# Optimization experiments

Hardware: AMD Instinct MI355X
Metric: run time of the kernel (lower is better)

The kernel has to match this reference:

```python
import jax, jax.numpy as jnp
import numpy as np
import math

B, S, D, H, L, V = 2, 2048, 1024, 16, 2, 32000
HD = D // H          # head_dim = 64
FF = 4 * D           # ffn hidden = 4096
NEG_INF = -1e9


def setup_inputs() -> dict:
    key = jax.random.key(0)
    ks = jax.random.split(key, 12)
    w = lambda k, shape: jax.random.normal(k, shape, dtype=jnp.float32) * 0.02
    return {
        "tokens": jax.random.randint(ks[0], (B, S), 0, V),
        "tok_emb": w(ks[1], (V, D)),
        "pos_emb": w(ks[2], (S, D)),
        # torch nn.Linear weights are [out, in]; stacked over layers
        "wq": w(ks[3], (L, D, D)),
        "wk": w(ks[4], (L, D, D)),
        "wv": w(ks[5], (L, D, D)),
        "wo": w(ks[6], (L, D, D)),
        "w1": w(ks[7], (L, FF, D)),
        "w2": w(ks[8], (L, D, FF)),
        "ln1_g": jnp.ones((L, D)), "ln1_b": jnp.zeros((L, D)),
        "ln2_g": jnp.ones((L, D)), "ln2_b": jnp.zeros((L, D)),
        "lnf_g": jnp.ones((D,)), "lnf_b": jnp.zeros((D,)),
        "w_out": w(ks[9], (V, D)),
    }


def _layernorm(x, g, b):
    m = jnp.mean(x, axis=-1, keepdims=True)
    v = jnp.mean(jnp.square(x - m), axis=-1, keepdims=True)
    return (x - m) * jax.lax.rsqrt(v + 1e-5) * g + b


def _transformer(tokens, tok_emb, pos_emb, wq, wk, wv, wo, w1, w2,
                 ln1_g, ln1_b, ln2_g, ln2_b, lnf_g, lnf_b, w_out):
    s = tokens.shape[1]
    # causal additive mask [1,1,S,S]
    mask = jnp.where(jnp.tril(jnp.ones((s, s), dtype=bool)), 0.0, NEG_INF)[None, None]
    h = tok_emb[tokens] + pos_emb[None, :s]
    scale = 1.0 / math.sqrt(HD)
    for l in range(L):
        # pre-norm attention
        a_in = _layernorm(h, ln1_g[l], ln1_b[l])
        q = (a_in @ wq[l].T).reshape(B, s, H, HD)
        k = (a_in @ wk[l].T).reshape(B, s, H, HD)
        v = (a_in @ wv[l].T).reshape(B, s, H, HD)
        scores = jnp.einsum('bqhd,bkhd->bhqk', q, k) * scale + mask
        attn = jax.nn.softmax(scores.astype(jnp.float32), axis=-1).astype(h.dtype)
        o = jnp.einsum('bhqk,bkhd->bqhd', attn, v).reshape(B, s, D)
        h = h + o @ wo[l].T
        # pre-norm ReLU FFN
        f_in = _layernorm(h, ln2_g[l], ln2_b[l])
        h = h + jax.nn.relu(f_in @ w1[l].T) @ w2[l].T
    h = _layernorm(h, lnf_g, lnf_b)
    return h @ w_out.T  # [B,S,V]


def reference(tokens, tok_emb, pos_emb, wq, wk, wv, wo, w1, w2,
              ln1_g, ln1_b, ln2_g, ln2_b, lnf_g, lnf_b, w_out):
    return _transformer(tokens, tok_emb, pos_emb, wq, wk, wv, wo, w1, w2,
                        ln1_g, ln1_b, ln2_g, ln2_b, lnf_g, lnf_b, w_out)
```

## Files before the change

### kernel.cpp

```cpp
#include <hip/hip_runtime.h>

#define Bv 2
#define Sv 2048
#define Dv 1024
#define Hv 16
#define HDv 64
#define FFv 4096
#define Vv 32000

typedef short bf16x8 __attribute__((ext_vector_type(8)));
typedef float f32x4 __attribute__((ext_vector_type(4)));
typedef unsigned short us8 __attribute__((ext_vector_type(8)));
typedef unsigned short us4 __attribute__((ext_vector_type(4)));
typedef unsigned short u16;

__device__ __forceinline__ u16 f2bf(float f) {
  union { float f; unsigned u; } x; x.f = f;
  x.u += 0x7fffu + ((x.u >> 16) & 1u);
  return (u16)(x.u >> 16);
}
__device__ __forceinline__ u16 f2bf_rtz(float f) {
  union { float f; unsigned u; } x; x.f = f;
  return (u16)(x.u >> 16);
}

__device__ __forceinline__ void gld16(const void* g, void* l) {
  __builtin_amdgcn_global_load_lds(
      (const __attribute__((address_space(1))) unsigned*)g,
      (__attribute__((address_space(3))) unsigned*)l, 16, 0, 0);
}

__global__ __launch_bounds__(256) void k_embed(const int* __restrict__ tok,
    const float* __restrict__ te, const float* __restrict__ pe,
    float* __restrict__ h) {
  int row = blockIdx.x;
  int s = row & (Sv - 1);
  int t = tok[row];
  float4 va = ((const float4*)(te + (size_t)t * Dv))[threadIdx.x];
  float4 vb = ((const float4*)(pe + (size_t)s * Dv))[threadIdx.x];
  float4 o;
  o.x = va.x + vb.x; o.y = va.y + vb.y; o.z = va.z + vb.z; o.w = va.w + vb.w;
  ((float4*)(h + (size_t)row * Dv))[threadIdx.x] = o;
}

__global__ __launch_bounds__(256) void k_cvt(const float* __restrict__ x,
    u16* __restrict__ y, int n4) {
  int i = blockIdx.x * 256 + threadIdx.x;
  if (i >= n4) return;
  float4 v = ((const float4*)x)[i];
  us4 o = { f2bf(v.x), f2bf(v.y), f2bf(v.z), f2bf(v.w) };
  ((us4*)y)[i] = o;
}

__global__ __launch_bounds__(256) void k_ln(const float* __restrict__ x,
    const float* __restrict__ g, const float* __restrict__ bb,
    u16* __restrict__ y) {
  int row = blockIdx.x, t = threadIdx.x;
  float4 v = ((const float4*)(x + (size_t)row * Dv))[t];
  float s = v.x + v.y + v.z + v.w;
#pragma unroll
  for (int m = 32; m; m >>= 1) s += __shfl_xor(s, m, 64);
  __shared__ float red[4];
  if ((t & 63) == 0) red[t >> 6] = s;
  __syncthreads();
  float mean = (red[0] + red[1] + red[2] + red[3]) * (1.0f / Dv);
  __syncthreads();
  float dx = v.x - mean, dy = v.y - mean, dz = v.z - mean, dw = v.w - mean;
  float s2 = dx * dx + dy * dy + dz * dz + dw * dw;
#pragma unroll
  for (int m = 32; m; m >>= 1) s2 += __shfl_xor(s2, m, 64);
  if ((t & 63) == 0) red[t >> 6] = s2;
  __syncthreads();
  float var = (red[0] + red[1] + red[2] + red[3]) * (1.0f / Dv);
  float rstd = rsqrtf(var + 1e-5f);
  float4 gg = ((const float4*)g)[t];
  float4 be = ((const float4*)bb)[t];
  us4 o = { f2bf(dx * rstd * gg.x + be.x), f2bf(dy * rstd * gg.y + be.y),
            f2bf(dz * rstd * gg.z + be.z), f2bf(dw * rstd * gg.w + be.w) };
  ((us4*)(y + (size_t)row * Dv))[t] = o;
}

__device__ __forceinline__ void stage32(const u16* __restrict__ g, int ldK,
    u16* lds, int row_base, int kt, int lane) {
  int row = row_base + (lane >> 2);
  int slot = (lane & 3) ^ ((row >> 1) & 3);
  const u16* src = g + (size_t)row * ldK + (kt << 5) + (slot << 3);
  gld16(src, lds + (row_base << 5));
}
__device__ __forceinline__ bf16x8 ldfragA(const u16* lds, int row, int ks) {
  return *(const bf16x8*)((const char*)lds + row * 64 + ((ks ^ ((row >> 1) & 3)) << 4));
}

__device__ __forceinline__ void stage64(const u16* __restrict__ g, int ldK,
    u16* lds, int row_base, int kt, int lane) {
  int row = row_base + (lane >> 3);
  int slot = (lane & 7) ^ (row & 7);
  const u16* src = g + (size_t)row * ldK + (kt << 6) + (slot << 3);
  gld16(src, lds + (row_base << 6));
}
__device__ __forceinline__ bf16x8 ldf64(const u16* lds, int row, int slot) {
  return *(const bf16x8*)((const char*)lds + row * 128 + ((slot ^ (row & 7)) << 4));
}

template <int EPI>
__global__ __launch_bounds__(512, 2) void k_256(const u16* __restrict__ A,
    const u16* __restrict__ Bm, const float* __restrict__ res,
    float* __restrict__ Cf, u16* __restrict__ Cb, int M, int N, int K) {
  __shared__ u16 As[2][256 * 64];
  __shared__ u16 Bs[2][256 * 64];
  int TM = M >> 8, TN = N >> 8, nwg = TM * TN;
  int orig = blockIdx.x;
  int qd = nwg >> 3, rm = nwg & 7, xcd = orig & 7;
  int wg = (xcd < rm ? xcd * (qd + 1) : rm * (qd + 1) + (xcd - rm) * qd) + (orig >> 3);
  int bm = wg % TM, bn = wg / TM;
  int m0 = bm << 8, n0 = bn << 8;
  int lane = threadIdx.x & 63, wid = threadIdx.x >> 6;
  int wr = wid >> 2, wc = wid & 3;
  int NT = K >> 6;
  const u16* Ag = A + (size_t)m0 * K;
  const u16* Bg = Bm + (size_t)n0 * K;
  int frow = lane & 15, ks = lane >> 4;

  f32x4 acc[8][4] = {};
  bf16x8 af[4], bk0[4], bk1[4];

#pragma unroll
  for (int tt = 0; tt < 2; tt++) {
#pragma unroll
    for (int j = 0; j < 4; j++) stage64(Ag, K, As[tt], wid * 32 + j * 8, tt, lane);
#pragma unroll
    for (int j = 0; j < 4; j++) stage64(Bg, K, Bs[tt], wid * 32 + j * 8, tt, lane);
  }
  asm volatile("s_waitcnt vmcnt(8)" ::: "memory");
  __builtin_amdgcn_s_barrier();

  for (int t = 0; t < NT; t++) {
    int p = t & 1;
    const u16* Ab = As[p];
    const u16* Bb = Bs[p];
#pragma unroll
    for (int f = 0; f < 4; f++) af[f] = ldf64(Ab, wr * 128 + f * 16 + frow, ks);
#pragma unroll
    for (int n = 0; n < 4; n++) bk0[n] = ldf64(Bb, wc * 64 + n * 16 + frow, ks);
    __builtin_amdgcn_s_barrier();
    asm volatile("s_waitcnt lgkmcnt(0)" ::: "memory");
    __builtin_amdgcn_sched_barrier(0);
    __builtin_amdgcn_s_setprio(1);
#pragma unroll
    for (int f = 0; f < 4; f++)
#pragma unroll
      for (int n = 0; n < 4; n++)
        acc[f][n] = __builtin_amdgcn_mfma_f32_16x16x32_bf16(af[f], bk0[n], acc[f][n], 0, 0, 0);
    __builtin_amdgcn_s_setprio(0);
    __builtin_amdgcn_sched_barrier(0);
    __builtin_amdgcn_s_barrier();
#pragma unroll
    for (int f = 0; f < 4; f++) af[f] = ldf64(Ab, wr * 128 + 64 + f * 16 + frow, ks);
#pragma unroll
    for (int n = 0; n < 4; n++) bk1[n] = ldf64(Bb, wc * 64 + n * 16 + frow, 4 + ks);
    __builtin_amdgcn_s_barrier();
    asm volatile("s_waitcnt lgkmcnt(0)" ::: "memory");
    __builtin_amdgcn_sched_barrier(0);
    __builtin_amdgcn_s_setprio(1);
#pragma unroll
    for (int f = 0; f < 4; f++)
#pragma unroll
      for (int n = 0; n < 4; n++)
        acc[4 + f][n] = __builtin_amdgcn_mfma_f32_16x16x32_bf16(af[f], bk0[n], acc[4 + f][n], 0, 0, 0);
    __builtin_amdgcn_s_setprio(0);
    __builtin_amdgcn_sched_barrier(0);
    __builtin_amdgcn_s_barrier();
#pragma unroll
    for (int f = 0; f < 4; f++) af[f] = ldf64(Ab, wr * 128 + f * 16 + frow, 4 + ks);
    __builtin_amdgcn_s_barrier();
    asm volatile("s_waitcnt lgkmcnt(0)" ::: "memory");
    __builtin_amdgcn_sched_barrier(0);
    __builtin_amdgcn_s_setprio(1);
#pragma unroll
    for (int f = 0; f < 4; f++)
#pragma unroll
      for (int n = 0; n < 4; n++)
        acc[f][n] = __builtin_amdgcn_mfma_f32_16x16x32_bf16(af[f], bk1[n], acc[f][n], 0, 0, 0);
    __builtin_amdgcn_s_setprio(0);
    __builtin_amdgcn_sched_barrier(0);
    __builtin_amdgcn_s_barrier();
#pragma unroll
    for (int f = 0; f < 4; f++) af[f] = ldf64(Ab, wr * 128 + 64 + f * 16 + frow, 4 + ks);
    __builtin_amdgcn_s_barrier();
    asm volatile("s_waitcnt lgkmcnt(0)" ::: "memory");
    __builtin_amdgcn_sched_barrier(0);
    __builtin_amdgcn_s_setprio(1);
#pragma unroll
    for (int f = 0; f < 4; f++)
#pragma unroll
      for (int n = 0; n < 4; n++)
        acc[4 + f][n] = __builtin_amdgcn_mfma_f32_16x16x32_bf16(af[f], bk1[n], acc[4 + f][n], 0, 0, 0);
    __builtin_amdgcn_s_setprio(0);
    __builtin_amdgcn_sched_barrier(0);
    __builtin_amdgcn_s_barrier();
    if (t + 2 < NT) {
#pragma unroll
      for (int j = 0; j < 4; j++) stage64(Ag, K, As[p], wid * 32 + j * 8, t + 2, lane);
#pragma unroll
      for (int j = 0; j < 4; j++) stage64(Bg, K, Bs[p], wid * 32 + j * 8, t + 2, lane);
      asm volatile("s_waitcnt vmcnt(8)" ::: "memory");
    } else {
      asm volatile("s_waitcnt vmcnt(0)" ::: "memory");
    }
    __builtin_amdgcn_s_barrier();
  }

#pragma unroll
  for (int f = 0; f < 8; f++) {
#pragma unroll
    for (int r = 0; r < 4; r++) {
      int row = m0 + wr * 128 + f * 16 + (lane >> 4) * 4 + r;
#pragma unroll
      for (int n = 0; n < 4; n++) {
        int col = n0 + wc * 64 + n * 16 + frow;
        float val = acc[f][n][r];
        size_t idx = (size_t)row * N + col;
        if constexpr (EPI == 1) { Cf[idx] = val + res[idx]; }
        else if constexpr (EPI == 0) { __builtin_nontemporal_store(val, &Cf[idx]); }
        else if constexpr (EPI == 2) { Cb[idx] = f2bf(val); }
        else { Cb[idx] = f2bf(fmaxf(val, 0.0f)); }
      }
    }
  }
}

template <int EPI>
__global__ __launch_bounds__(512, 4) void k_gemm8(const u16* __restrict__ A,
    const u16* __restrict__ Bm, const float* __restrict__ res,
    float* __restrict__ Cf, u16* __restrict__ Cb, int M, int N, int K) {
  __shared__ u16 As[2][128 * 32];
  __shared__ u16 Bs[2][256 * 32];
  int TM = M >> 7, TN = N >> 8, nwg = TM * TN;
  int orig = blockIdx.x;
  int qd = nwg >> 3, rm = nwg & 7, xcd = orig & 7;
  int wg = (xcd < rm ? xcd * (qd + 1) : rm * (qd + 1) + (xcd - rm) * qd) + (orig >> 3);
  int bm = wg % TM, bn = wg / TM;
  int m0 = bm << 7, n0 = bn << 8;
  int lane = threadIdx.x & 63, wid = threadIdx.x >> 6;
  int wr = wid >> 2, wc = wid & 3;
  int NT = K >> 5;
  const u16* Ag = A + (size_t)m0 * K;
  const u16* Bg = Bm + (size_t)n0 * K;
  int frow = lane & 15, ks = lane >> 4;

  f32x4 acc[4][4] = {};
  bf16x8 af[4], bf[4];

#pragma unroll
  for (int tt = 0; tt < 2; tt++) {
    stage32(Ag, K, As[tt], wid * 16, tt, lane);
    stage32(Bg, K, Bs[tt], wid * 32, tt, lane);
    stage32(Bg, K, Bs[tt], wid * 32 + 16, tt, lane);
  }
  asm volatile("s_waitcnt vmcnt(3)" ::: "memory");
  __builtin_amdgcn_s_barrier();

  for (int t = 0; t < NT; t++) {
    int p = t & 1;
    const u16* Ab = As[p];
    const u16* Bb = Bs[p];
#pragma unroll
    for (int f = 0; f < 4; f++) af[f] = ldfragA(Ab, wr * 64 + f * 16 + frow, ks);
#pragma unroll
    for (int n = 0; n < 4; n++) bf[n] = ldfragA(Bb, wc * 64 + n * 16 + frow, ks);
    __builtin_amdgcn_s_barrier();
    asm volatile("s_waitcnt lgkmcnt(0)" ::: "memory");
    __builtin_amdgcn_sched_barrier(0);
    __builtin_amdgcn_s_setprio(1);
#pragma unroll
    for (int f = 0; f < 2; f++)
#pragma unroll
      for (int n = 0; n < 4; n++)
        acc[f][n] = __builtin_amdgcn_mfma_f32_16x16x32_bf16(af[f], bf[n], acc[f][n], 0, 0, 0);
    __builtin_amdgcn_s_setprio(0);
    __builtin_amdgcn_sched_barrier(0);
    __builtin_amdgcn_s_barrier();
    if (t < NT - 2) {
      stage32(Ag, K, As[p], wid * 16, t + 2, lane);
      stage32(Bg, K, Bs[p], wid * 32, t + 2, lane);
      stage32(Bg, K, Bs[p], wid * 32 + 16, t + 2, lane);
    }
    __builtin_amdgcn_s_setprio(1);
#pragma unroll
    for (int f = 0; f < 2; f++)
#pragma unroll
      for (int n = 0; n < 4; n++)
        acc[2 + f][n] = __builtin_amdgcn_mfma_f32_16x16x32_bf16(af[2 + f], bf[n], acc[2 + f][n], 0, 0, 0);
    __builtin_amdgcn_s_setprio(0);
    __builtin_amdgcn_sched_barrier(0);
    if (t < NT - 2) { asm volatile("s_waitcnt vmcnt(3)" ::: "memory"); }
    else            { asm volatile("s_waitcnt vmcnt(0)" ::: "memory"); }
    __builtin_amdgcn_s_barrier();
  }

#pragma unroll
  for (int f = 0; f < 4; f++) {
#pragma unroll
    for (int r = 0; r < 4; r++) {
      int row = m0 + wr * 64 + f * 16 + (lane >> 4) * 4 + r;
#pragma unroll
      for (int n = 0; n < 4; n++) {
        int col = n0 + wc * 64 + n * 16 + frow;
        float val = acc[f][n][r];
        size_t idx = (size_t)row * N + col;
        if constexpr (EPI == 1) { Cf[idx] = val + res[idx]; }
        else if constexpr (EPI == 0) { __builtin_nontemporal_store(val, &Cf[idx]); }
        else if constexpr (EPI == 2) { Cb[idx] = f2bf(val); }
        else { Cb[idx] = f2bf(fmaxf(val, 0.0f)); }
      }
    }
  }
}

template <int EPI>
__global__ __launch_bounds__(256, 4) void k_gemmv(const u16* __restrict__ A,
    const u16* __restrict__ Bm, const float* __restrict__ res,
    float* __restrict__ Cf, u16* __restrict__ Cb, int M, int N, int K) {
  __shared__ u16 As[2][128 * 32];
  __shared__ u16 Bs[2][128 * 32];
  int TM = M >> 7, TN = N >> 7, nwg = TM * TN;
  int orig = blockIdx.x;
  int qd = nwg >> 3, rm = nwg & 7, xcd = orig & 7;
  int wg = (xcd < rm ? xcd * (qd + 1) : rm * (qd + 1) + (xcd - rm) * qd) + (orig >> 3);
  int bm = wg % TM, bn = wg / TM;
  int m0 = bm << 7, n0 = bn << 7;
  int lane = threadIdx.x & 63, wid = threadIdx.x >> 6;
  int wr = wid >> 1, wc = wid & 1;
  int NT = K >> 5;
  const u16* Ag = A + (size_t)m0 * K;
  const u16* Bg = Bm + (size_t)n0 * K;
  int frow = lane & 15, ks = lane >> 4;

  f32x4 acc[4][4] = {};
  bf16x8 af[4], bf[4];

#pragma unroll
  for (int tt = 0; tt < 2; tt++) {
    stage32(Ag, K, As[tt], wid * 32, tt, lane);
    stage32(Ag, K, As[tt], wid * 32 + 16, tt, lane);
    stage32(Bg, K, Bs[tt], wid * 32, tt, lane);
    stage32(Bg, K, Bs[tt], wid * 32 + 16, tt, lane);
  }
  asm volatile("s_waitcnt vmcnt(4)" ::: "memory");
  __builtin_amdgcn_s_barrier();

  for (int t = 0; t < NT; t++) {
    int p = t & 1;
    const u16* Ab = As[p];
    const u16* Bb = Bs[p];
#pragma unroll
    for (int f = 0; f < 4; f++) af[f] = ldfragA(Ab, wr * 64 + f * 16 + frow, ks);
#pragma unroll
    for (int n = 0; n < 4; n++) bf[n] = ldfragA(Bb, wc * 64 + n * 16 + frow, ks);
    __builtin_amdgcn_s_barrier();
    asm volatile("s_waitcnt lgkmcnt(0)" ::: "memory");
    __builtin_amdgcn_sched_barrier(0);
    __builtin_amdgcn_s_setprio(1);
#pragma unroll
    for (int f = 0; f < 2; f++)
#pragma unroll
      for (int n = 0; n < 4; n++)
        acc[f][n] = __builtin_amdgcn_mfma_f32_16x16x32_bf16(af[f], bf[n], acc[f][n], 0, 0, 0);
    __builtin_amdgcn_s_setprio(0);
    __builtin_amdgcn_sched_barrier(0);
    __builtin_amdgcn_s_barrier();
    if (t < NT - 2) {
      stage32(Ag, K, As[p], wid * 32, t + 2, lane);
      stage32(Ag, K, As[p], wid * 32 + 16, t + 2, lane);
      stage32(Bg, K, Bs[p], wid * 32, t + 2, lane);
      stage32(Bg, K, Bs[p], wid * 32 + 16, t + 2, lane);
    }
    __builtin_amdgcn_s_setprio(1);
#pragma unroll
    for (int f = 0; f < 2; f++)
#pragma unroll
      for (int n = 0; n < 4; n++)
        acc[2 + f][n] = __builtin_amdgcn_mfma_f32_16x16x32_bf16(af[2 + f], bf[n], acc[2 + f][n], 0, 0, 0);
    __builtin_amdgcn_s_setprio(0);
    __builtin_amdgcn_sched_barrier(0);
    if (t < NT - 2) { asm volatile("s_waitcnt vmcnt(4)" ::: "memory"); }
    else            { asm volatile("s_waitcnt vmcnt(0)" ::: "memory"); }
    __builtin_amdgcn_s_barrier();
  }

#pragma unroll
  for (int f = 0; f < 4; f++) {
#pragma unroll
    for (int r = 0; r < 4; r++) {
      int row = m0 + wr * 64 + f * 16 + (lane >> 4) * 4 + r;
#pragma unroll
      for (int n = 0; n < 4; n++) {
        int col = n0 + wc * 64 + n * 16 + frow;
        float val = acc[f][n][r];
        size_t idx = (size_t)row * N + col;
        if constexpr (EPI == 1) { Cf[idx] = val + res[idx]; }
        else if constexpr (EPI == 0) { __builtin_nontemporal_store(val, &Cf[idx]); }
        else if constexpr (EPI == 2) { Cb[idx] = f2bf(val); }
        else { Cb[idx] = f2bf(fmaxf(val, 0.0f)); }
      }
    }
  }
}

__global__ __launch_bounds__(256) void k_transpose(const u16* __restrict__ v,
    u16* __restrict__ vt, int stride) {
  int st = blockIdx.x & 31;
  int bh = blockIdx.x >> 5;
  int b = bh >> 4, hh = bh & 15;
  __shared__ u16 tile[64][72];
  int t = threadIdx.x;
  int rr = t >> 3, cc = (t & 7) << 3;
#pragma unroll
  for (int it = 0; it < 2; it++) {
    int r = rr + it * 32;
    us8 val = *(const us8*)(v + (size_t)(b * Sv + st * 64 + r) * stride + hh * HDv + cc);
    *(us8*)&tile[r][cc] = val;
  }
  __syncthreads();
#pragma unroll
  for (int it = 0; it < 2; it++) {
    int d = rr + it * 32;
    us8 val;
#pragma unroll
    for (int j = 0; j < 8; j++) val[j] = tile[cc + j][d];
    *(us8*)(vt + ((size_t)bh * HDv + d) * Sv + st * 64 + cc) = val;
  }
}

__global__ __launch_bounds__(256) void k_attn(const u16* __restrict__ qg,
    const u16* __restrict__ kg, const u16* __restrict__ vt,
    u16* __restrict__ og) {
  int qt = blockIdx.x & 15;
  int bh = blockIdx.x >> 4;
  int b = bh >> 4, hh = bh & 15;
  int wv = threadIdx.x >> 6, lane = threadIdx.x & 63;
  int q0 = qt * 128 + wv * 32;
  __shared__ u16 plds_s[4][32 * 40];
  __shared__ float alds_s[4][2][16];
  u16* plds = plds_s[wv];
  float (*alds)[16] = alds_s[wv];
  const int QS = 3 * Dv;
  const float scale = 0.125f;
  int qcol = lane & 15, g = lane >> 4;

  bf16x8 qf[2][2];
#pragma unroll
  for (int fm = 0; fm < 2; fm++)
#pragma unroll
    for (int dh = 0; dh < 2; dh++)
      qf[fm][dh] = *(const bf16x8*)(qg + (size_t)(b * Sv + q0 + fm * 16 + qcol) * QS
                                    + hh * HDv + dh * 32 + g * 8);

  f32x4 oacc[2][4] = {};
  float mrun[2] = { -1e30f, -1e30f };
  float lrun[2] = { 0.0f, 0.0f };

  int ktmax = (q0 + 31) >> 5;
  for (int kt = 0; kt <= ktmax; kt++) {
    int k0 = kt * 32;
    bf16x8 kf[2][2];
#pragma unroll
    for (int kn = 0; kn < 2; kn++)
#pragma unroll
      for (int dh = 0; dh < 2; dh++)
        kf[kn][dh] = *(const bf16x8*)(kg + (size_t)(b * Sv + k0 + kn * 16 + qcol) * QS
                                      + hh * HDv + dh * 32 + g * 8);
    f32x4 sa[2][2] = {};
#pragma unroll
    for (int dh = 0; dh < 2; dh++)
#pragma unroll
      for (int fm = 0; fm < 2; fm++)
#pragma unroll
        for (int kn = 0; kn < 2; kn++)
          sa[fm][kn] = __builtin_amdgcn_mfma_f32_16x16x32_bf16(kf[kn][dh], qf[fm][dh], sa[fm][kn], 0, 0, 0);

    bool full = (k0 + 31 <= q0);
#pragma unroll
    for (int fm = 0; fm < 2; fm++) {
      int qrow = q0 + fm * 16 + qcol;
      float s[2][4];
#pragma unroll
      for (int kn = 0; kn < 2; kn++)
#pragma unroll
        for (int r = 0; r < 4; r++) {
          float v = sa[fm][kn][r] * scale;
          if (!full && (k0 + kn * 16 + g * 4 + r) > qrow) v = -1e30f;
          s[kn][r] = v;
        }
      float rmx = s[0][0];
#pragma unroll
      for (int kn = 0; kn < 2; kn++)
#pragma unroll
        for (int r = 0; r < 4; r++) rmx = fmaxf(rmx, s[kn][r]);
      rmx = fmaxf(rmx, __shfl_xor(rmx, 16, 64));
      rmx = fmaxf(rmx, __shfl_xor(rmx, 32, 64));
      float nm;
      if (__all(rmx - mrun[fm] <= 8.0f)) {
        nm = mrun[fm];
      } else {
        nm = fmaxf(mrun[fm], rmx);
        float alpha = __expf(mrun[fm] - nm);
        mrun[fm] = nm;
        lrun[fm] *= alpha;
        if (g == 0) alds[fm][qcol] = alpha;
#pragma unroll
        for (int r = 0; r < 4; r++) {
          float al = alds[fm][g * 4 + r];
#pragma unroll
          for (int dn = 0; dn < 4; dn++) oacc[fm][dn][r] *= al;
        }
      }
      float rs = 0.0f;
      float pv[2][4];
#pragma unroll
      for (int kn = 0; kn < 2; kn++)
#pragma unroll
        for (int r = 0; r < 4; r++) { pv[kn][r] = __expf(s[kn][r] - nm); rs += pv[kn][r]; }
      rs += __shfl_xor(rs, 16, 64);
      rs += __shfl_xor(rs, 32, 64);
      lrun[fm] += rs;
#pragma unroll
      for (int kn = 0; kn < 2; kn++) {
        us4 pk = { f2bf_rtz(pv[kn][0]), f2bf_rtz(pv[kn][1]),
                   f2bf_rtz(pv[kn][2]), f2bf_rtz(pv[kn][3]) };
        *(us4*)(plds + (fm * 16 + qcol) * 40 + kn * 16 + g * 4) = pk;
      }
    }
    bf16x8 pf[2];
#pragma unroll
    for (int fm = 0; fm < 2; fm++)
      pf[fm] = *(const bf16x8*)(plds + (fm * 16 + qcol) * 40 + g * 8);
    bf16x8 vf[4];
#pragma unroll
    for (int dn = 0; dn < 4; dn++)
      vf[dn] = *(const bf16x8*)(vt + ((size_t)bh * HDv + dn * 16 + qcol) * Sv
                                + k0 + g * 8);
#pragma unroll
    for (int fm = 0; fm < 2; fm++)
#pragma unroll
      for (int dn = 0; dn < 4; dn++)
        oacc[fm][dn] = __builtin_amdgcn_mfma_f32_16x16x32_bf16(pf[fm], vf[dn], oacc[fm][dn], 0, 0, 0);
  }

#pragma unroll
  for (int fm = 0; fm < 2; fm++)
    if (g == 0) alds[fm][qcol] = 1.0f / lrun[fm];
#pragma unroll
  for (int fm = 0; fm < 2; fm++)
#pragma unroll
    for (int r = 0; r < 4; r++) {
      float li = alds[fm][g * 4 + r];
      int row = q0 + fm * 16 + g * 4 + r;
#pragma unroll
      for (int dn = 0; dn < 4; dn++)
        og[(size_t)(b * Sv + row) * Dv + hh * HDv + dn * 16 + qcol] =
            f2bf(oacc[fm][dn][r] * li);
    }
}

extern "C" void kernel_launch(void* const* d_in, const int* in_sizes, int n_in,
                              void* d_out, int out_size, void* d_ws, size_t ws_size,
                              hipStream_t stream) {
  const int*   tok  = (const int*)d_in[0];
  const float* te   = (const float*)d_in[1];
  const float* pe   = (const float*)d_in[2];
  const float* wq   = (const float*)d_in[3];
  const float* wk   = (const float*)d_in[4];
  const float* wvv  = (const float*)d_in[5];
  const float* wo   = (const float*)d_in[6];
  const float* w1   = (const float*)d_in[7];
  const float* w2   = (const float*)d_in[8];
  const float* ln1g = (const float*)d_in[9];
  const float* ln1b = (const float*)d_in[10];
  const float* ln2g = (const float*)d_in[11];
  const float* ln2b = (const float*)d_in[12];
  const float* lnfg = (const float*)d_in[13];
  const float* lnfb = (const float*)d_in[14];
  const float* wout = (const float*)d_in[15];
  float* out = (float*)d_out;

  char* p = (char*)d_ws;
  float* h  = (float*)p; p += (size_t)4096 * 1024 * 4;
  u16* a    = (u16*)p;   p += (size_t)4096 * 1024 * 2;
  u16* qkv  = (u16*)p;   p += (size_t)4096 * 3072 * 2;
  u16* vt   = (u16*)p;   p += (size_t)32 * 64 * 2048 * 2;
  u16* o    = (u16*)p;   p += (size_t)4096 * 1024 * 2;
  u16* f1   = (u16*)p;   p += (size_t)4096 * 4096 * 2;
  u16* wb   = (u16*)p;   p += (size_t)32000 * 1024 * 2;

  const int M = Bv * Sv;

  k_embed<<<M, 256, 0, stream>>>(tok, te, pe, h);
  for (int l = 0; l < 2; l++) {
    k_ln<<<M, 256, 0, stream>>>(h, ln1g + l * Dv, ln1b + l * Dv, a);
    k_cvt<<<1024, 256, 0, stream>>>(wq  + (size_t)l * Dv * Dv, wb,              (Dv * Dv) / 4);
    k_cvt<<<1024, 256, 0, stream>>>(wk  + (size_t)l * Dv * Dv, wb + Dv * Dv,    (Dv * Dv) / 4);
    k_cvt<<<1024, 256, 0, stream>>>(wvv + (size_t)l * Dv * Dv, wb + 2 * Dv * Dv,(Dv * Dv) / 4);
    k_gemm8<2><<<32 * 12, 512, 0, stream>>>(a, wb, nullptr, nullptr, qkv, M, 3 * Dv, Dv);
    k_transpose<<<1024, 256, 0, stream>>>(qkv + 2 * Dv, vt, 3 * Dv);
    k_attn<<<512, 256, 0, stream>>>(qkv, qkv + Dv, vt, o);
    k_cvt<<<1024, 256, 0, stream>>>(wo + (size_t)l * Dv * Dv, wb, (Dv * Dv) / 4);
    k_gemmv<1><<<32 * 8, 256, 0, stream>>>(o, wb, h, h, nullptr, M, Dv, Dv);
    k_ln<<<M, 256, 0, stream>>>(h, ln2g + l * Dv, ln2b + l * Dv, a);
    k_cvt<<<4096, 256, 0, stream>>>(w1 + (size_t)l * FFv * Dv, wb, (FFv * Dv) / 4);
    k_256<3><<<16 * 16, 512, 0, stream>>>(a, wb, nullptr, nullptr, f1, M, FFv, Dv);
    k_cvt<<<4096, 256, 0, stream>>>(w2 + (size_t)l * Dv * FFv, wb, (Dv * FFv) / 4);
    k_gemmv<1><<<32 * 8, 256, 0, stream>>>(f1, wb, h, h, nullptr, M, Dv, FFv);
  }
  k_ln<<<M, 256, 0, stream>>>(h, lnfg, lnfb, a);
  k_cvt<<<32000, 256, 0, stream>>>(wout, wb, (Vv * Dv) / 4);
  k_256<0><<<16 * 125, 512, 0, stream>>>(a, wb, nullptr, out, nullptr, M, Vv, Dv);
}
```

Before: 1.075 ms.

## Restructure 256x256 GEMM main loop to batch LDS reads and prefetch earlier

The per-tile loop of the large bf16 GEMM (used for the FFN up-projection and the vocabulary projection) is rewritten. Most LDS fragment loads for all four MFMA sub-blocks are now issued up front into separate registers, and most intermediate workgroup barriers are removed. The global prefetch of tile t+2 is moved before the last MFMA block so that it overlaps with compute. The aim is to cut barrier and LDS-latency stalls, at the cost of many more live fragment registers, which may add register pressure or spills under launch_bounds(512,2).

```diff
diff --git a/kernel.cpp b/kernel.cpp
--- a/kernel.cpp
+++ b/kernel.cpp
@@ -103,7 +103,7 @@
 }
 
 template <int EPI>
-__global__ __launch_bounds__(512, 2) void k_256(const u16* __restrict__ A,
+__global__ __launch_bounds__(512, 2) void k_pipe(const u16* __restrict__ A,
     const u16* __restrict__ Bm, const float* __restrict__ res,
     float* __restrict__ Cf, u16* __restrict__ Cb, int M, int N, int K) {
   __shared__ u16 As[2][256 * 64];
@@ -122,7 +122,7 @@
   int frow = lane & 15, ks = lane >> 4;
 
   f32x4 acc[8][4] = {};
-  bf16x8 af[4], bk0[4], bk1[4];
+  bf16x8 af0[4], af1[4], af2[4], af3[4], bf0[4], bf1[4];
 
 #pragma unroll
   for (int tt = 0; tt < 2; tt++) {
@@ -139,74 +139,57 @@
     const u16* Ab = As[p];
     const u16* Bb = Bs[p];
 #pragma unroll
-    for (int f = 0; f < 4; f++) af[f] = ldf64(Ab, wr * 128 + f * 16 + frow, ks);
-#pragma unroll
-    for (int n = 0; n < 4; n++) bk0[n] = ldf64(Bb, wc * 64 + n * 16 + frow, ks);
-    __builtin_amdgcn_s_barrier();
+    for (int f = 0; f < 4; f++) af0[f] = ldf64(Ab, wr * 128 + f * 16 + frow, ks);
+#pragma unroll
+    for (int n = 0; n < 4; n++) bf0[n] = ldf64(Bb, wc * 64 + n * 16 + frow, ks);
+#pragma unroll
+    for (int f = 0; f < 4; f++) af1[f] = ldf64(Ab, wr * 128 + 64 + f * 16 + frow, ks);
+#pragma unroll
+    for (int n = 0; n < 4; n++) bf1[n] = ldf64(Bb, wc * 64 + n * 16 + frow, 4 + ks);
+#pragma unroll
+    for (int f = 0; f < 4; f++) af2[f] = ldf64(Ab, wr * 128 + f * 16 + frow, 4 + ks);
+    __builtin_amdgcn_s_setprio(1);
+#pragma unroll
+    for (int f = 0; f < 4; f++)
+#pragma unroll
+      for (int n = 0; n < 4; n++)
+        acc[f][n] = __builtin_amdgcn_mfma_f32_16x16x32_bf16(af0[f], bf0[n], acc[f][n], 0, 0, 0);
+    __builtin_amdgcn_s_setprio(0);
+    __builtin_amdgcn_s_setprio(1);
+#pragma unroll
+    for (int f = 0; f < 4; f++)
+#pragma unroll
+      for (int n = 0; n < 4; n++)
+        acc[4 + f][n] = __builtin_amdgcn_mfma_f32_16x16x32_bf16(af1[f], bf0[n], acc[4 + f][n], 0, 0, 0);
+    __builtin_amdgcn_s_setprio(0);
+#pragma unroll
+    for (int f = 0; f < 4; f++) af3[f] = ldf64(Ab, wr * 128 + 64 + f * 16 + frow, 4 + ks);
+    __builtin_amdgcn_s_setprio(1);
+#pragma unroll
+    for (int f = 0; f < 4; f++)
+#pragma unroll
+      for (int n = 0; n < 4; n++)
+        acc[f][n] = __builtin_amdgcn_mfma_f32_16x16x32_bf16(af2[f], bf1[n], acc[f][n], 0, 0, 0);
+    __builtin_amdgcn_s_setprio(0);
     asm volatile("s_waitcnt lgkmcnt(0)" ::: "memory");
     __builtin_amdgcn_sched_barrier(0);
+    __builtin_amdgcn_s_barrier();
+    if (t + 2 < NT) {
+#pragma unroll
+      for (int j = 0; j < 4; j++) stage64(Ag, K, As[p], wid * 32 + j * 8, t + 2, lane);
+#pragma unroll
+      for (int j = 0; j < 4; j++) stage64(Bg, K, Bs[p], wid * 32 + j * 8, t + 2, lane);
+    }
     __builtin_amdgcn_s_setprio(1);
 #pragma unroll
     for (int f = 0; f < 4; f++)
 #pragma unroll
       for (int n = 0; n < 4; n++)
-        acc[f][n] = __builtin_amdgcn_mfma_f32_16x16x32_bf16(af[f], bk0[n], acc[f][n], 0, 0, 0);
-    __builtin_amdgcn_s_setprio(0);
-    __builtin_amdgcn_sched_barrier(0);
-    __builtin_amdgcn_s_barrier();
-#pragma unroll
-    for (int f = 0; f < 4; f++) af[f] = ldf64(Ab, wr * 128 + 64 + f * 16 + frow, ks);
-#pragma unroll
-    for (int n = 0; n < 4; n++) bk1[n] = ldf64(Bb, wc * 64 + n * 16 + frow, 4 + ks);
-    __builtin_amdgcn_s_barrier();
-    asm volatile("s_waitcnt lgkmcnt(0)" ::: "memory");
-    __builtin_amdgcn_sched_barrier(0);
-    __builtin_amdgcn_s_setprio(1);
-#pragma unroll
-    for (int f = 0; f < 4; f++)
-#pragma unroll
-      for (int n = 0; n < 4; n++)
-        acc[4 + f][n] = __builtin_amdgcn_mfma_f32_16x16x32_bf16(af[f], bk0[n], acc[4 + f][n], 0, 0, 0);
-    __builtin_amdgcn_s_setprio(0);
-    __builtin_amdgcn_sched_barrier(0);
-    __builtin_amdgcn_s_barrier();
-#pragma unroll
-    for (int f = 0; f < 4; f++) af[f] = ldf64(Ab, wr * 128 + f * 16 + frow, 4 + ks);
-    __builtin_amdgcn_s_barrier();
-    asm volatile("s_waitcnt lgkmcnt(0)" ::: "memory");
-    __builtin_amdgcn_sched_barrier(0);
-    __builtin_amdgcn_s_setprio(1);
-#pragma unroll
-    for (int f = 0; f < 4; f++)
-#pragma unroll
-      for (int n = 0; n < 4; n++)
-        acc[f][n] = __builtin_amdgcn_mfma_f32_16x16x32_bf16(af[f], bk1[n], acc[f][n], 0, 0, 0);
-    __builtin_amdgcn_s_setprio(0);
-    __builtin_amdgcn_sched_barrier(0);
-    __builtin_amdgcn_s_barrier();
-#pragma unroll
-    for (int f = 0; f < 4; f++) af[f] = ldf64(Ab, wr * 128 + 64 + f * 16 + frow, 4 + ks);
-    __builtin_amdgcn_s_barrier();
-    asm volatile("s_waitcnt lgkmcnt(0)" ::: "memory");
-    __builtin_amdgcn_sched_barrier(0);
-    __builtin_amdgcn_s_setprio(1);
-#pragma unroll
-    for (int f = 0; f < 4; f++)
-#pragma unroll
-      for (int n = 0; n < 4; n++)
-        acc[4 + f][n] = __builtin_amdgcn_mfma_f32_16x16x32_bf16(af[f], bk1[n], acc[4 + f][n], 0, 0, 0);
-    __builtin_amdgcn_s_setprio(0);
-    __builtin_amdgcn_sched_barrier(0);
-    __builtin_amdgcn_s_barrier();
-    if (t + 2 < NT) {
-#pragma unroll
-      for (int j = 0; j < 4; j++) stage64(Ag, K, As[p], wid * 32 + j * 8, t + 2, lane);
-#pragma unroll
-      for (int j = 0; j < 4; j++) stage64(Bg, K, Bs[p], wid * 32 + j * 8, t + 2, lane);
-      asm volatile("s_waitcnt vmcnt(8)" ::: "memory");
-    } else {
-      asm volatile("s_waitcnt vmcnt(0)" ::: "memory");
-    }
+        acc[4 + f][n] = __builtin_amdgcn_mfma_f32_16x16x32_bf16(af3[f], bf1[n], acc[4 + f][n], 0, 0, 0);
+    __builtin_amdgcn_s_setprio(0);
+    __builtin_amdgcn_sched_barrier(0);
+    if (t + 2 < NT) { asm volatile("s_waitcnt vmcnt(8)" ::: "memory"); }
+    else            { asm volatile("s_waitcnt vmcnt(0)" ::: "memory"); }
     __builtin_amdgcn_s_barrier();
   }
 
@@ -608,11 +591,11 @@
     k_gemmv<1><<<32 * 8, 256, 0, stream>>>(o, wb, h, h, nullptr, M, Dv, Dv);
     k_ln<<<M, 256, 0, stream>>>(h, ln2g + l * Dv, ln2b + l * Dv, a);
     k_cvt<<<4096, 256, 0, stream>>>(w1 + (size_t)l * FFv * Dv, wb, (FFv * Dv) / 4);
-    k_256<3><<<16 * 16, 512, 0, stream>>>(a, wb, nullptr, nullptr, f1, M, FFv, Dv);
+    k_pipe<3><<<16 * 16, 512, 0, stream>>>(a, wb, nullptr, nullptr, f1, M, FFv, Dv);
     k_cvt<<<4096, 256, 0, stream>>>(w2 + (size_t)l * Dv * FFv, wb, (Dv * FFv) / 4);
     k_gemmv<1><<<32 * 8, 256, 0, stream>>>(f1, wb, h, h, nullptr, M, Dv, FFv);
   }
   k_ln<<<M, 256, 0, stream>>>(h, lnfg, lnfb, a);
   k_cvt<<<32000, 256, 0, stream>>>(wout, wb, (Vv * Dv) / 4);
-  k_256<0><<<16 * 125, 512, 0, stream>>>(a, wb, nullptr, out, nullptr, M, Vv, Dv);
-}
+  k_pipe<0><<<16 * 125, 512, 0, stream>>>(a, wb, nullptr, out, nullptr, M, Vv, Dv);
+}
```

Result: faster. 1.006 ms (-6.4%).
